# Kernel tuning notes

Hardware: AMD Instinct MI355X
Metric: run time of the kernel (lower is better)

The kernel has to match this reference:

```python
import jax, jax.numpy as jnp
import numpy as np

B, N, D_IN, D, K, H, ITERS = 128, 4096, 64, 64, 8, 128, 3
SCALE = D ** -0.5
EPS_ATTN = 1e-8
EPS_LN = 1e-5


def layer_norm(x, g, b):
    m = jnp.mean(x, axis=-1, keepdims=True)
    v = jnp.mean((x - m) ** 2, axis=-1, keepdims=True)
    return (x - m) * jax.lax.rsqrt(v + EPS_LN) * g + b


def setup_inputs() -> dict:
    key = jax.random.key(0)
    ks = jax.random.split(key, 16)
    s = 0.05
    return {
        "inputs": jax.random.normal(ks[0], (B, N, D_IN), dtype=jnp.float32),
        "noise": jax.random.normal(ks[1], (B, K, D), dtype=jnp.float32),
        "slots_mu": jax.random.normal(ks[2], (1, 1, D), dtype=jnp.float32),
        "slots_sigma": jax.random.normal(ks[3], (1, 1, D), dtype=jnp.float32),
        "Wq": jax.random.normal(ks[4], (D, D), dtype=jnp.float32) * s,
        "Wk": jax.random.normal(ks[5], (D_IN, D), dtype=jnp.float32) * s,
        "Wv": jax.random.normal(ks[6], (D_IN, D), dtype=jnp.float32) * s,
        "W_ih": jax.random.normal(ks[7], (3 * D, D), dtype=jnp.float32) * s,
        "W_hh": jax.random.normal(ks[8], (3 * D, D), dtype=jnp.float32) * s,
        "b_ih": jnp.zeros((3 * D,), dtype=jnp.float32),
        "b_hh": jnp.zeros((3 * D,), dtype=jnp.float32),
        "mlp_W1": jax.random.normal(ks[9], (D, H), dtype=jnp.float32) * s,
        "mlp_b1": jnp.zeros((H,), dtype=jnp.float32),
        "mlp_W2": jax.random.normal(ks[10], (H, D), dtype=jnp.float32) * s,
        "mlp_b2": jnp.zeros((D,), dtype=jnp.float32),
        "ln_in_g": jnp.ones((D_IN,), dtype=jnp.float32),
        "ln_in_b": jnp.zeros((D_IN,), dtype=jnp.float32),
        "ln_s_g": jnp.ones((D,), dtype=jnp.float32),
        "ln_s_b": jnp.zeros((D,), dtype=jnp.float32),
        "ln_ff_g": jnp.ones((D,), dtype=jnp.float32),
        "ln_ff_b": jnp.zeros((D,), dtype=jnp.float32),
    }


def reference(inputs, noise, slots_mu, slots_sigma, Wq, Wk, Wv,
              W_ih, W_hh, b_ih, b_hh, mlp_W1, mlp_b1, mlp_W2, mlp_b2,
              ln_in_g, ln_in_b, ln_s_g, ln_s_b, ln_ff_g, ln_ff_b):
    # slots = Normal(mu, sigma) with externally supplied standard noise
    slots = slots_mu + slots_sigma * noise                      # [B,K,D]
    x = layer_norm(inputs, ln_in_g, ln_in_b)                     # [B,N,D_IN]
    k = x @ Wk                                                   # [B,N,D]
    v = x @ Wv                                                   # [B,N,D]

    for _ in range(ITERS):
        slots_prev = slots
        s = layer_norm(slots, ln_s_g, ln_s_b)
        q = s @ Wq                                               # [B,K,D]
        dots = jnp.einsum('bid,bjd->bij', q, k) * SCALE          # [B,K,N]
        attn = jax.nn.softmax(dots, axis=1) + EPS_ATTN           # softmax over slots
        attn_n = attn / jnp.sum(attn, axis=-1, keepdims=True)
        updates = jnp.einsum('bjd,bij->bid', v, attn_n)          # [B,K,D]

        # single-step GRU (torch nn.GRU gate order: reset, update, new)
        gx = updates @ W_ih.T + b_ih                             # [B,K,3D]
        gh = slots_prev @ W_hh.T + b_hh                          # [B,K,3D]
        gx_r, gx_z, gx_n = jnp.split(gx, 3, axis=-1)
        gh_r, gh_z, gh_n = jnp.split(gh, 3, axis=-1)
        r = jax.nn.sigmoid(gx_r + gh_r)
        z = jax.nn.sigmoid(gx_z + gh_z)
        n = jnp.tanh(gx_n + r * gh_n)
        slots = (1.0 - z) * n + z * slots_prev

        slots = layer_norm(slots, ln_ff_g, ln_ff_b)
        slots = slots + (jax.nn.relu(slots @ mlp_W1 + mlp_b1) @ mlp_W2 + mlp_b2)
    return slots
```

## Files before the change

kernel.cpp:

```cpp
#include <hip/hip_runtime.h>
#include <hip/hip_bf16.h>

typedef unsigned int u32;
typedef unsigned short u16;
typedef __attribute__((ext_vector_type(8))) short short8;
typedef __attribute__((ext_vector_type(4))) float f32x4;
typedef __attribute__((ext_vector_type(2))) u32 u32x2;

#define B_      128
#define N_      4096
#define K_      8
#define ITERS_  3
#define OC_     8
#define CPB_    4
#define CHUNK   128
#define SCALE_  0.125f
#define EPS_A   1e-8f
#define EPS_LN  1e-5f

__device__ __forceinline__ float bf_lo(u32 u){ union{u32 v; float f;} x; x.v = u<<16; return x.f; }
__device__ __forceinline__ u16 f2bf(float f){
  union{float f; u32 v;} x; x.f = f;
  u32 v = x.v;
  return (u16)((v + 0x7fffu + ((v>>16)&1u))>>16);
}
__device__ __forceinline__ float wsum64(float v){
  #pragma unroll
  for (int off=32; off; off>>=1) v += __shfl_xor(v, off, 64);
  return v;
}
__device__ __forceinline__ void gll16(const void* g, void* l){
  __builtin_amdgcn_global_load_lds(
      (const __attribute__((address_space(1))) void*)g,
      (__attribute__((address_space(3))) void*)l, 16, 0, 0);
}

__global__ void prep_t(const float* __restrict__ Wih, const float* __restrict__ Whh,
                       const float* __restrict__ Wq,  const float* __restrict__ Wk,
                       float* __restrict__ WihT, float* __restrict__ WhhT,
                       float* __restrict__ Wqk){
  int t = threadIdx.x;
  if (blockIdx.x < 48){
    int idx = blockIdx.x*256 + t;
    int g = idx>>6, d = idx&63;
    WihT[d*192+g] = Wih[idx];
    WhhT[d*192+g] = Whh[idx];
  } else {
    __shared__ float WkL[64*65];
    int bi = blockIdx.x - 48;
    #pragma unroll
    for (int k=0;k<16;++k){
      int idx = t + k*256;
      int d = idx>>6, m = idx&63;
      WkL[m*65+d] = Wk[idx];
    }
    __syncthreads();
    int a = bi*4 + (t>>6), d = t&63;
    float acc = 0.f;
    #pragma unroll 8
    for (int m=0;m<64;++m) acc += Wq[a*64+m]*WkL[m*65+d];
    Wqk[a*64+d] = acc;
  }
}

__global__ __launch_bounds__(512) void slots_init(
    const float* __restrict__ noise, const float* __restrict__ mu, const float* __restrict__ sigma,
    const float* __restrict__ Wqk,
    const float* __restrict__ lnsg, const float* __restrict__ lnsb,
    float* __restrict__ slots, u16* __restrict__ qbuf16){
  int b = blockIdx.x, t = threadIdx.x;
  int i = t>>6, d = t&63;
  __shared__ float svL[K_][68];
  float s0 = mu[d] + sigma[d]*noise[b*512 + t];
  slots[b*512 + t] = s0;
  float m  = wsum64(s0) * (1.f/64.f);
  float df = s0 - m;
  float vv = wsum64(df*df) * (1.f/64.f);
  float sv = df * rsqrtf(vv + EPS_LN) * lnsg[d] + lnsb[d];
  svL[i][d] = sv;
  __syncthreads();
  float qt = 0.f;
  #pragma unroll 8
  for (int dd=0; dd<64; ++dd) qt += svL[i][dd] * Wqk[dd*64 + d];
  qbuf16[b*1024 + t] = f2bf(qt);
  qbuf16[b*1024 + 512 + t] = 0;
}

template<int FUSED>
__global__ __launch_bounds__(256,4) void bigpass(
    const float* __restrict__ inp, u16* __restrict__ xhat,
    const u16* __restrict__ qbuf16,
    const float* __restrict__ lng, const float* __restrict__ lnb,
    float* __restrict__ PU, float* __restrict__ PS){
  int b = blockIdx.y, oc = blockIdx.x, t = threadIdx.x;
  int w = t>>6, lane = t&63;
  int fr = lane&15, fq = lane>>4;

  __shared__ __align__(16) char smem[38912];
  char* qA   = smem + 32768;
  char* abuf = smem + 34816;
  __shared__ float SL[4][8];
  u32 smb = (u32)(size_t)smem;

  if (t < 128){
    uint4 v = ((const uint4*)(qbuf16 + b*1024))[t];
    int row = t>>3;
    *(uint4*)(qA + ((t*16) ^ ((row&7)<<4))) = v;
  }
  long tile0 = ((long)b*OC_ + oc)*CPB_;
  long base_pos = (long)b*N_ + (long)oc*(CPB_*CHUNK);

  short8 qf0, qf1;
  f32x4 c2 = (f32x4){0.f,0.f,0.f,0.f};
  float tsl[4] = {0.f,0.f,0.f,0.f};

  float lg[16], lb[16];
  if (FUSED){
    int q = t&3;
    #pragma unroll
    for (int e=0;e<16;++e){ lg[e] = lng[q*16+e]; lb[e] = lnb[q*16+e]; }
  }
  if (!FUSED){
    const char* gsrc = (const char*)xhat + (tile0<<14) + w*4096 + lane*16;
    char* ldst = smem + w*4096;
    #pragma unroll
    for (int j=0;j<4;++j) gll16(gsrc + j*1024, ldst + j*1024);
  }

  #pragma unroll
  for (int cc=0; cc<CPB_; ++cc){
    int buf = cc&1;
    if (FUSED){
      #pragma unroll
      for (int p2=0;p2<2;++p2){
        int r = p2*64 + (t>>2), q = t&3;
        const float4* xr = (const float4*)(inp + (base_pos + (long)cc*CHUNK + r)*64 + q*16);
        float xv[16]; float s=0.f, sq=0.f;
        #pragma unroll
        for (int c=0;c<4;++c){
          float4 f = xr[c];
          xv[c*4+0]=f.x; xv[c*4+1]=f.y; xv[c*4+2]=f.z; xv[c*4+3]=f.w;
          s  += f.x+f.y+f.z+f.w;
          sq += f.x*f.x+f.y*f.y+f.z*f.z+f.w*f.w;
        }
        s  += __shfl_xor(s,1,64);  s  += __shfl_xor(s,2,64);
        sq += __shfl_xor(sq,1,64); sq += __shfl_xor(sq,2,64);
        float mean = s*(1.f/64.f);
        float inv  = rsqrtf(sq*(1.f/64.f) - mean*mean + EPS_LN);
        u32 pk[8];
        #pragma unroll
        for (int e=0;e<8;++e){
          float a0 = (xv[e*2]  -mean)*inv*lg[e*2]   + lb[e*2];
          float a1 = (xv[e*2+1]-mean)*inv*lg[e*2+1] + lb[e*2+1];
          pk[e] = (u32)f2bf(a0) | ((u32)f2bf(a1)<<16);
        }
        uint4 v0; v0.x=pk[0]; v0.y=pk[1]; v0.z=pk[2]; v0.w=pk[3];
        uint4 v1; v1.x=pk[4]; v1.y=pk[5]; v1.z=pk[6]; v1.w=pk[7];
        int byte0 = ((r>>5)<<12) | (q<<10) | (((r>>2)&1)<<9) | (((r>>3)&3)<<7) | ((r&3)<<5);
        *(uint4*)(smem + buf*16384 + byte0)      = v0;
        *(uint4*)(smem + buf*16384 + byte0 + 16) = v1;
      }
    }
    __syncthreads();
    if (FUSED){
      const uint4* ls = (const uint4*)(smem + buf*16384);
      uint4* gim = (uint4*)((char*)xhat + ((tile0+cc)<<14));
      #pragma unroll
      for (int j=0;j<4;++j) gim[t + j*256] = ls[t + j*256];
    } else if (cc+1 < CPB_){
      const char* gsrc = (const char*)xhat + ((tile0+cc+1)<<14) + w*4096 + lane*16;
      char* ldst = smem + (buf^1)*16384 + w*4096;
      #pragma unroll
      for (int j=0;j<4;++j) gll16(gsrc + j*1024, ldst + j*1024);
    }
    if (cc==0){
      qf0 = *(const short8*)(qA + ((fr*128 +  0 + fq*16) ^ ((fr&7)<<4)));
      qf1 = *(const short8*)(qA + ((fr*128 + 64 + fq*16) ^ ((fr&7)<<4)));
    }
    f32x4 c1[2];
    #pragma unroll
    for (int nt=0;nt<2;++nt){
      c1[nt] = (f32x4){0.f,0.f,0.f,0.f};
      #pragma unroll
      for (int kk=0;kk<2;++kk){
        int byte = (w<<12) | ((kk*2+(fq>>1))<<10) | (((fr>>2)&1)<<9)
                 | ((nt*2+(fr>>3))<<7) | ((fr&3)<<5) | ((fq&1)<<4);
        short8 xf = *(const short8*)(smem + buf*16384 + byte);
        c1[nt] = __builtin_amdgcn_mfma_f32_16x16x32_bf16(kk?qf1:qf0, xf, c1[nt], 0,0,0);
      }
    }
    #pragma unroll
    for (int nt=0;nt<2;++nt){
      float d0 = c1[nt][0]*SCALE_, d1 = c1[nt][1]*SCALE_;
      float d2 = c1[nt][2]*SCALE_, d3 = c1[nt][3]*SCALE_;
      float m = fmaxf(fmaxf(d0,d1), fmaxf(d2,d3));
      m = fmaxf(m, __shfl_xor(m, 16, 64));
      float e0 = __expf(d0-m), e1 = __expf(d1-m), e2 = __expf(d2-m), e3 = __expf(d3-m);
      float sl = e0+e1+e2+e3;
      float inv = 1.f/(sl + __shfl_xor(sl, 16, 64));
      float a0 = e0*inv + EPS_A, a1 = e1*inv + EPS_A;
      float a2 = e2*inv + EPS_A, a3 = e3*inv + EPS_A;
      tsl[0]+=a0; tsl[1]+=a1; tsl[2]+=a2; tsl[3]+=a3;
      int pos2 = w*64 + nt*32 + fr*2;
      #pragma unroll
      for (int r=0;r<4;++r){
        int slot = fq*4 + r;
        float av = (r==0)?a0:((r==1)?a1:((r==2)?a2:a3));
        int byteA = ((slot<<8) + pos2) ^ ((slot&7)<<4);
        *(u16*)(abuf + byteA) = f2bf(av);
      }
    }
    __syncthreads();
    {
      u32 va = smb + buf*16384 + (w<<10) + (fq<<7) + (fr<<1);
      u32x2 tv0,tv1,tv2,tv3,tv4,tv5,tv6,tv7;
      asm volatile("ds_read_b64_tr_b16 %0, %1 offset:0"     : "=v"(tv0) : "v"(va));
      asm volatile("ds_read_b64_tr_b16 %0, %1 offset:512"   : "=v"(tv1) : "v"(va));
      asm volatile("ds_read_b64_tr_b16 %0, %1 offset:4096"  : "=v"(tv2) : "v"(va));
      asm volatile("ds_read_b64_tr_b16 %0, %1 offset:4608"  : "=v"(tv3) : "v"(va));
      asm volatile("ds_read_b64_tr_b16 %0, %1 offset:8192"  : "=v"(tv4) : "v"(va));
      asm volatile("ds_read_b64_tr_b16 %0, %1 offset:8704"  : "=v"(tv5) : "v"(va));
      asm volatile("ds_read_b64_tr_b16 %0, %1 offset:12288" : "=v"(tv6) : "v"(va));
      asm volatile("ds_read_b64_tr_b16 %0, %1 offset:12800" : "=v"(tv7) : "v"(va));
      short8 pa[4];
      #pragma unroll
      for (int k2=0;k2<4;++k2){
        int byteP = (fr<<8) + ((k2*64 + fq*16) ^ ((fr&7)<<4));
        pa[k2] = *(const short8*)(abuf + byteP);
      }
      asm volatile("s_waitcnt lgkmcnt(0)" ::: "memory");
      __builtin_amdgcn_sched_barrier(0);
      union { short8 s8; u32 u4[4]; } xb;
      xb.u4[0]=tv0.x; xb.u4[1]=tv0.y; xb.u4[2]=tv1.x; xb.u4[3]=tv1.y;
      c2 = __builtin_amdgcn_mfma_f32_16x16x32_bf16(pa[0], xb.s8, c2, 0,0,0);
      xb.u4[0]=tv2.x; xb.u4[1]=tv2.y; xb.u4[2]=tv3.x; xb.u4[3]=tv3.y;
      c2 = __builtin_amdgcn_mfma_f32_16x16x32_bf16(pa[1], xb.s8, c2, 0,0,0);
      xb.u4[0]=tv4.x; xb.u4[1]=tv4.y; xb.u4[2]=tv5.x; xb.u4[3]=tv5.y;
      c2 = __builtin_amdgcn_mfma_f32_16x16x32_bf16(pa[2], xb.s8, c2, 0,0,0);
      xb.u4[0]=tv6.x; xb.u4[1]=tv6.y; xb.u4[2]=tv7.x; xb.u4[3]=tv7.y;
      c2 = __builtin_amdgcn_mfma_f32_16x16x32_bf16(pa[3], xb.s8, c2, 0,0,0);
    }
  }
  long pb = ((long)b*OC_ + oc)*512;
  if (fq < 2){
    #pragma unroll
    for (int r=0;r<4;++r)
      PU[pb + (fq*4+r)*64 + w*16 + fr] = c2[r];
  }
  #pragma unroll
  for (int mk=1; mk<16; mk<<=1){
    tsl[0] += __shfl_xor(tsl[0], mk, 64);
    tsl[1] += __shfl_xor(tsl[1], mk, 64);
    tsl[2] += __shfl_xor(tsl[2], mk, 64);
    tsl[3] += __shfl_xor(tsl[3], mk, 64);
  }
  if (fr==0 && fq<2){
    SL[w][fq*4+0]=tsl[0]; SL[w][fq*4+1]=tsl[1];
    SL[w][fq*4+2]=tsl[2]; SL[w][fq*4+3]=tsl[3];
  }
  __syncthreads();
  if (t < 8)
    PS[((long)b*OC_ + oc)*8 + t] = SL[0][t]+SL[1][t]+SL[2][t]+SL[3][t];
}

__global__ __launch_bounds__(512,2) void slot_update(
    const float* __restrict__ PU, const float* __restrict__ PS,
    float* __restrict__ slots,
    const float* __restrict__ WihT, const float* __restrict__ WhhT,
    const float* __restrict__ bih, const float* __restrict__ bhh,
    const float* __restrict__ W1, const float* __restrict__ b1,
    const float* __restrict__ W2, const float* __restrict__ b2,
    const float* __restrict__ lnffg, const float* __restrict__ lnffb,
    const float* __restrict__ lnsg, const float* __restrict__ lnsb,
    const float* __restrict__ Wv, const float* __restrict__ Wqk,
    u16* __restrict__ qbuf16, float* __restrict__ dout, int last){
  extern __shared__ float wls[];
  __shared__ float updL[K_][68];
  __shared__ float spL[K_][68];
  __shared__ float sfL[K_][68];
  __shared__ float hL[K_][132];
  int b = blockIdx.x, t = threadIdx.x;
  int i = t>>6, d = t&63;
  float u=0.f;
  #pragma unroll
  for (int c=0;c<OC_;++c) u += PU[((long)b*OC_ + c)*512 + t];
  float S=0.f;
  #pragma unroll
  for (int c=0;c<OC_;++c) S += PS[((long)b*OC_ + c)*8 + i];
  float ut = u / S;
  float sp = slots[b*512 + t];
  sfL[i][d] = ut;
  spL[i][d] = sp;
  {
    const float4* wa = (const float4*)WihT;
    #pragma unroll
    for (int k2=0;k2<6;++k2){ int idx = t + k2*512; ((float4*)wls)[idx] = wa[idx]; }
  }
  __syncthreads();
  float upd = 0.f;
  #pragma unroll 8
  for (int dd=0; dd<64; ++dd) upd += sfL[i][dd]*Wv[dd*64 + d];
  updL[i][d] = upd;
  __syncthreads();
  float gx0 = bih[d], gx1 = bih[64+d], gx2 = bih[128+d];
  #pragma unroll 8
  for (int dd=0; dd<64; ++dd){
    float uv = updL[i][dd];
    gx0 += uv*wls[dd*192 + d];
    gx1 += uv*wls[dd*192 + 64 + d];
    gx2 += uv*wls[dd*192 + 128 + d];
  }
  __syncthreads();
  {
    const float4* wb = (const float4*)WhhT;
    #pragma unroll
    for (int k2=0;k2<6;++k2){ int idx = t + k2*512; ((float4*)wls)[idx] = wb[idx]; }
  }
  __syncthreads();
  float gh0 = bhh[d], gh1 = bhh[64+d], gh2 = bhh[128+d];
  #pragma unroll 8
  for (int dd=0; dd<64; ++dd){
    float sv = spL[i][dd];
    gh0 += sv*wls[dd*192 + d];
    gh1 += sv*wls[dd*192 + 64 + d];
    gh2 += sv*wls[dd*192 + 128 + d];
  }
  float rg = 1.f/(1.f+__expf(-(gx0+gh0)));
  float zg = 1.f/(1.f+__expf(-(gx1+gh1)));
  float ng = tanhf(gx2 + rg*gh2);
  float sn = (1.f-zg)*ng + zg*sp;
  float m1 = wsum64(sn)*(1.f/64.f);
  float df = sn-m1;
  float vv = wsum64(df*df)*(1.f/64.f);
  float sf = df*rsqrtf(vv+EPS_LN)*lnffg[d] + lnffb[d];
  sfL[i][d] = sf;
  __syncthreads();
  float h0 = b1[d], h1 = b1[64+d];
  #pragma unroll 8
  for (int dd=0;dd<64;++dd){
    float sv = sfL[i][dd];
    h0 += sv*W1[dd*128 + d];
    h1 += sv*W1[dd*128 + 64 + d];
  }
  h0 = fmaxf(h0, 0.f); h1 = fmaxf(h1, 0.f);
  hL[i][d] = h0; hL[i][d+64] = h1;
  __syncthreads();
  float o = b2[d];
  #pragma unroll 8
  for (int hh=0; hh<128; ++hh) o += hL[i][hh]*W2[hh*64 + d];
  float out = sf + o;
  slots[b*512 + t] = out;
  if (last){
    dout[b*512 + t] = out;
  } else {
    float m2 = wsum64(out)*(1.f/64.f);
    float d2 = out-m2;
    float v2 = wsum64(d2*d2)*(1.f/64.f);
    float sq = d2*rsqrtf(v2+EPS_LN)*lnsg[d] + lnsb[d];
    updL[i][d] = sq;
    __syncthreads();
    float qt=0.f;
    #pragma unroll 8
    for (int dd=0;dd<64;++dd) qt += updL[i][dd]*Wqk[dd*64 + d];
    qbuf16[b*1024 + t] = f2bf(qt);
    qbuf16[b*1024 + 512 + t] = 0;
  }
}

extern "C" void kernel_launch(void* const* d_in, const int* in_sizes, int n_in,
                              void* d_out, int out_size, void* d_ws, size_t ws_size,
                              hipStream_t stream){
  const float* inp   = (const float*)d_in[0];
  const float* noise = (const float*)d_in[1];
  const float* mu    = (const float*)d_in[2];
  const float* sigma = (const float*)d_in[3];
  const float* Wq    = (const float*)d_in[4];
  const float* Wk    = (const float*)d_in[5];
  const float* Wv    = (const float*)d_in[6];
  const float* Wih   = (const float*)d_in[7];
  const float* Whh   = (const float*)d_in[8];
  const float* bih   = (const float*)d_in[9];
  const float* bhh   = (const float*)d_in[10];
  const float* W1    = (const float*)d_in[11];
  const float* b1    = (const float*)d_in[12];
  const float* W2    = (const float*)d_in[13];
  const float* b2    = (const float*)d_in[14];
  const float* lnig  = (const float*)d_in[15];
  const float* lnib  = (const float*)d_in[16];
  const float* lnsg  = (const float*)d_in[17];
  const float* lnsb  = (const float*)d_in[18];
  const float* lnffg = (const float*)d_in[19];
  const float* lnffb = (const float*)d_in[20];
  float* out = (float*)d_out;

  char* ws = (char*)d_ws;
  u16*   xhat   = (u16*)(ws);
  u16*   qbuf16 = (u16*)(ws + 67108864);
  float* slots  = (float*)(ws + 67371008);
  float* PU     = (float*)(ws + 67633152);
  float* PS     = (float*)(ws + 69730304);
  float* WihT   = (float*)(ws + 69763072);
  float* WhhT   = (float*)(ws + 69812224);
  float* Wqk    = (float*)(ws + 69861376);

  prep_t<<<64,256,0,stream>>>(Wih, Whh, Wq, Wk, WihT, WhhT, Wqk);
  slots_init<<<B_,512,0,stream>>>(noise, mu, sigma, Wqk, lnsg, lnsb, slots, qbuf16);
  for (int it=0; it<ITERS_; ++it){
    if (it==0)
      bigpass<1><<<dim3(OC_,B_),256,0,stream>>>(inp, xhat, qbuf16, lnig, lnib, PU, PS);
    else
      bigpass<0><<<dim3(OC_,B_),256,0,stream>>>(inp, xhat, qbuf16, lnig, lnib, PU, PS);
    slot_update<<<B_,512,49152,stream>>>(PU, PS, slots, WihT, WhhT, bih, bhh,
                                     W1, b1, W2, b2, lnffg, lnffb, lnsg, lnsb,
                                     Wv, Wqk, qbuf16, out, (it==ITERS_-1)?1:0);
  }
}
```

Baseline: 160.0 us.

## Make each wavefront own its own position chunks, removing block-wide barriers

```diff
diff --git a/kernel.cpp b/kernel.cpp
--- a/kernel.cpp
+++ b/kernel.cpp
@@ -11,9 +11,7 @@
 #define N_      4096
 #define K_      8
 #define ITERS_  3
-#define OC_     8
-#define CPB_    4
-#define CHUNK   128
+#define NW_     32
 #define SCALE_  0.125f
 #define EPS_A   1e-8f
 #define EPS_LN  1e-5f
@@ -95,97 +93,104 @@
   int b = blockIdx.y, oc = blockIdx.x, t = threadIdx.x;
   int w = t>>6, lane = t&63;
   int fr = lane&15, fq = lane>>4;
-
-  __shared__ __align__(16) char smem[38912];
-  char* qA   = smem + 32768;
-  char* abuf = smem + 34816;
-  __shared__ float SL[4][8];
-  u32 smb = (u32)(size_t)smem;
-
-  if (t < 128){
-    uint4 v = ((const uint4*)(qbuf16 + b*1024))[t];
-    int row = t>>3;
-    *(uint4*)(qA + ((t*16) ^ ((row&7)<<4))) = v;
-  }
-  long tile0 = ((long)b*OC_ + oc)*CPB_;
-  long base_pos = (long)b*N_ + (long)oc*(CPB_*CHUNK);
-
-  short8 qf0, qf1;
-  f32x4 c2 = (f32x4){0.f,0.f,0.f,0.f};
+  int wv = oc*4 + w;
+
+  __shared__ __align__(16) char smem[36864];
+  char* wbase = smem + w*9216;
+  char* abuf  = wbase + 8192;
+  u32 smb = (u32)(size_t)wbase;
+
+  long tile0 = (long)b*128 + wv*4;
+
+  const u16* qb = qbuf16 + b*1024;
+  short8 qf0 = *(const short8*)(qb + fr*64 +      fq*8);
+  short8 qf1 = *(const short8*)(qb + fr*64 + 32 + fq*8);
+
+  f32x4 c2[4];
+  #pragma unroll
+  for (int i=0;i<4;++i) c2[i] = (f32x4){0.f,0.f,0.f,0.f};
   float tsl[4] = {0.f,0.f,0.f,0.f};
 
-  float lg[16], lb[16];
-  if (FUSED){
-    int q = t&3;
-    #pragma unroll
-    for (int e=0;e<16;++e){ lg[e] = lng[q*16+e]; lb[e] = lnb[q*16+e]; }
-  }
   if (!FUSED){
-    const char* gsrc = (const char*)xhat + (tile0<<14) + w*4096 + lane*16;
-    char* ldst = smem + w*4096;
-    #pragma unroll
-    for (int j=0;j<4;++j) gll16(gsrc + j*1024, ldst + j*1024);
+    const char* g0 = (const char*)xhat + (tile0<<12) + lane*16;
+    #pragma unroll
+    for (int j=0;j<4;++j) gll16(g0 + j*1024, wbase + j*1024);
   }
 
   #pragma unroll
-  for (int cc=0; cc<CPB_; ++cc){
-    int buf = cc&1;
-    if (FUSED){
-      #pragma unroll
-      for (int p2=0;p2<2;++p2){
-        int r = p2*64 + (t>>2), q = t&3;
-        const float4* xr = (const float4*)(inp + (base_pos + (long)cc*CHUNK + r)*64 + q*16);
-        float xv[16]; float s=0.f, sq=0.f;
+  for (int cc=0; cc<4; ++cc){
+    int buf = FUSED ? 0 : (cc&1);
+    char* ibuf = wbase + buf*4096;
+    if (!FUSED){
+      if (cc < 3){
+        const char* gn = (const char*)xhat + ((tile0+cc+1)<<12) + lane*16;
+        char* ln = wbase + ((cc+1)&1)*4096;
         #pragma unroll
-        for (int c=0;c<4;++c){
-          float4 f = xr[c];
-          xv[c*4+0]=f.x; xv[c*4+1]=f.y; xv[c*4+2]=f.z; xv[c*4+3]=f.w;
-          s  += f.x+f.y+f.z+f.w;
-          sq += f.x*f.x+f.y*f.y+f.z*f.z+f.w*f.w;
-        }
-        s  += __shfl_xor(s,1,64);  s  += __shfl_xor(s,2,64);
-        sq += __shfl_xor(sq,1,64); sq += __shfl_xor(sq,2,64);
-        float mean = s*(1.f/64.f);
-        float inv  = rsqrtf(sq*(1.f/64.f) - mean*mean + EPS_LN);
-        u32 pk[8];
+        for (int j=0;j<4;++j) gll16(gn + j*1024, ln + j*1024);
+        asm volatile("s_waitcnt vmcnt(4)" ::: "memory");
+      } else {
+        asm volatile("s_waitcnt vmcnt(0)" ::: "memory");
+      }
+      __builtin_amdgcn_sched_barrier(0);
+    } else {
+      int r = lane>>1, h = lane&1;
+      const float4* xr = (const float4*)(inp + ((long)b*N_ + wv*128 + cc*32 + r)*64 + h*32);
+      float xv[32]; float s=0.f, sq=0.f;
+      #pragma unroll
+      for (int c=0;c<8;++c){
+        float4 f = xr[c];
+        xv[c*4+0]=f.x; xv[c*4+1]=f.y; xv[c*4+2]=f.z; xv[c*4+3]=f.w;
+        s  += f.x+f.y+f.z+f.w;
+        sq += f.x*f.x+f.y*f.y+f.z*f.z+f.w*f.w;
+      }
+      s  += __shfl_xor(s,1,64);
+      sq += __shfl_xor(sq,1,64);
+      float mean = s*(1.f/64.f);
+      float inv  = rsqrtf(sq*(1.f/64.f) - mean*mean + EPS_LN);
+      float lgv[32], lbv[32];
+      {
+        const float4* g4 = (const float4*)(lng + h*32);
+        const float4* b4 = (const float4*)(lnb + h*32);
         #pragma unroll
         for (int e=0;e<8;++e){
-          float a0 = (xv[e*2]  -mean)*inv*lg[e*2]   + lb[e*2];
-          float a1 = (xv[e*2+1]-mean)*inv*lg[e*2+1] + lb[e*2+1];
-          pk[e] = (u32)f2bf(a0) | ((u32)f2bf(a1)<<16);
+          float4 gv = g4[e], bv = b4[e];
+          lgv[e*4+0]=gv.x; lgv[e*4+1]=gv.y; lgv[e*4+2]=gv.z; lgv[e*4+3]=gv.w;
+          lbv[e*4+0]=bv.x; lbv[e*4+1]=bv.y; lbv[e*4+2]=bv.z; lbv[e*4+3]=bv.w;
         }
-        uint4 v0; v0.x=pk[0]; v0.y=pk[1]; v0.z=pk[2]; v0.w=pk[3];
-        uint4 v1; v1.x=pk[4]; v1.y=pk[5]; v1.z=pk[6]; v1.w=pk[7];
-        int byte0 = ((r>>5)<<12) | (q<<10) | (((r>>2)&1)<<9) | (((r>>3)&3)<<7) | ((r&3)<<5);
-        *(uint4*)(smem + buf*16384 + byte0)      = v0;
-        *(uint4*)(smem + buf*16384 + byte0 + 16) = v1;
-      }
-    }
-    __syncthreads();
-    if (FUSED){
-      const uint4* ls = (const uint4*)(smem + buf*16384);
-      uint4* gim = (uint4*)((char*)xhat + ((tile0+cc)<<14));
-      #pragma unroll
-      for (int j=0;j<4;++j) gim[t + j*256] = ls[t + j*256];
-    } else if (cc+1 < CPB_){
-      const char* gsrc = (const char*)xhat + ((tile0+cc+1)<<14) + w*4096 + lane*16;
-      char* ldst = smem + (buf^1)*16384 + w*4096;
-      #pragma unroll
-      for (int j=0;j<4;++j) gll16(gsrc + j*1024, ldst + j*1024);
-    }
-    if (cc==0){
-      qf0 = *(const short8*)(qA + ((fr*128 +  0 + fq*16) ^ ((fr&7)<<4)));
-      qf1 = *(const short8*)(qA + ((fr*128 + 64 + fq*16) ^ ((fr&7)<<4)));
-    }
+      }
+      u32 pk[16];
+      #pragma unroll
+      for (int e=0;e<16;++e){
+        float a0 = (xv[e*2]  -mean)*inv*lgv[e*2]   + lbv[e*2];
+        float a1 = (xv[e*2+1]-mean)*inv*lgv[e*2+1] + lbv[e*2+1];
+        pk[e] = (u32)f2bf(a0) | ((u32)f2bf(a1)<<16);
+      }
+      int pbits = (((r>>2)&1)<<9) | (((r>>3)&3)<<7) | ((r&3)<<5);
+      #pragma unroll
+      for (int half=0; half<2; ++half){
+        int dt = h*2 + half;
+        uint4 v0; v0.x=pk[half*8+0]; v0.y=pk[half*8+1]; v0.z=pk[half*8+2]; v0.w=pk[half*8+3];
+        uint4 v1; v1.x=pk[half*8+4]; v1.y=pk[half*8+5]; v1.z=pk[half*8+6]; v1.w=pk[half*8+7];
+        *(uint4*)(ibuf + ((dt<<10) | pbits))      = v0;
+        *(uint4*)(ibuf + ((dt<<10) | pbits) + 16) = v1;
+      }
+      asm volatile("s_waitcnt lgkmcnt(0)" ::: "memory");
+      __builtin_amdgcn_sched_barrier(0);
+      char* gim = (char*)xhat + ((tile0+cc)<<12) + lane*16;
+      #pragma unroll
+      for (int j=0;j<4;++j)
+        *(uint4*)(gim + j*1024) = *(const uint4*)(ibuf + lane*16 + j*1024);
+    }
+
     f32x4 c1[2];
     #pragma unroll
     for (int nt=0;nt<2;++nt){
       c1[nt] = (f32x4){0.f,0.f,0.f,0.f};
       #pragma unroll
       for (int kk=0;kk<2;++kk){
-        int byte = (w<<12) | ((kk*2+(fq>>1))<<10) | (((fr>>2)&1)<<9)
+        int byte = ((kk*2+(fq>>1))<<10) | (((fr>>2)&1)<<9)
                  | ((nt*2+(fr>>3))<<7) | ((fr&3)<<5) | ((fq&1)<<4);
-        short8 xf = *(const short8*)(smem + buf*16384 + byte);
+        short8 xf = *(const short8*)(ibuf + byte);
         c1[nt] = __builtin_amdgcn_mfma_f32_16x16x32_bf16(kk?qf1:qf0, xf, c1[nt], 0,0,0);
       }
     }
@@ -201,51 +206,47 @@
       float a0 = e0*inv + EPS_A, a1 = e1*inv + EPS_A;
       float a2 = e2*inv + EPS_A, a3 = e3*inv + EPS_A;
       tsl[0]+=a0; tsl[1]+=a1; tsl[2]+=a2; tsl[3]+=a3;
-      int pos2 = w*64 + nt*32 + fr*2;
-      #pragma unroll
-      for (int r=0;r<4;++r){
-        int slot = fq*4 + r;
-        float av = (r==0)?a0:((r==1)?a1:((r==2)?a2:a3));
-        int byteA = ((slot<<8) + pos2) ^ ((slot&7)<<4);
-        *(u16*)(abuf + byteA) = f2bf(av);
-      }
-    }
-    __syncthreads();
+      int pos2 = (nt*16 + fr)*2;
+      *(u16*)(abuf + (((fq*4+0)*64 + pos2) ^ (0<<4))) = f2bf(a0);
+      *(u16*)(abuf + (((fq*4+1)*64 + pos2) ^ (1<<4))) = f2bf(a1);
+      *(u16*)(abuf + (((fq*4+2)*64 + pos2) ^ (2<<4))) = f2bf(a2);
+      *(u16*)(abuf + (((fq*4+3)*64 + pos2) ^ (3<<4))) = f2bf(a3);
+    }
+    asm volatile("s_waitcnt lgkmcnt(0)" ::: "memory");
+    __builtin_amdgcn_sched_barrier(0);
     {
-      u32 va = smb + buf*16384 + (w<<10) + (fq<<7) + (fr<<1);
+      short8 pa = *(const short8*)(abuf + ((fr*64 + fq*16) ^ ((fr&3)<<4)));
+      u32 va = smb + buf*4096 + (fq<<7) + (fr<<1);
       u32x2 tv0,tv1,tv2,tv3,tv4,tv5,tv6,tv7;
-      asm volatile("ds_read_b64_tr_b16 %0, %1 offset:0"     : "=v"(tv0) : "v"(va));
-      asm volatile("ds_read_b64_tr_b16 %0, %1 offset:512"   : "=v"(tv1) : "v"(va));
-      asm volatile("ds_read_b64_tr_b16 %0, %1 offset:4096"  : "=v"(tv2) : "v"(va));
-      asm volatile("ds_read_b64_tr_b16 %0, %1 offset:4608"  : "=v"(tv3) : "v"(va));
-      asm volatile("ds_read_b64_tr_b16 %0, %1 offset:8192"  : "=v"(tv4) : "v"(va));
-      asm volatile("ds_read_b64_tr_b16 %0, %1 offset:8704"  : "=v"(tv5) : "v"(va));
-      asm volatile("ds_read_b64_tr_b16 %0, %1 offset:12288" : "=v"(tv6) : "v"(va));
-      asm volatile("ds_read_b64_tr_b16 %0, %1 offset:12800" : "=v"(tv7) : "v"(va));
-      short8 pa[4];
-      #pragma unroll
-      for (int k2=0;k2<4;++k2){
-        int byteP = (fr<<8) + ((k2*64 + fq*16) ^ ((fr&7)<<4));
-        pa[k2] = *(const short8*)(abuf + byteP);
-      }
+      asm volatile("ds_read_b64_tr_b16 %0, %1 offset:0"    : "=v"(tv0) : "v"(va));
+      asm volatile("ds_read_b64_tr_b16 %0, %1 offset:512"  : "=v"(tv1) : "v"(va));
+      asm volatile("ds_read_b64_tr_b16 %0, %1 offset:1024" : "=v"(tv2) : "v"(va));
+      asm volatile("ds_read_b64_tr_b16 %0, %1 offset:1536" : "=v"(tv3) : "v"(va));
+      asm volatile("ds_read_b64_tr_b16 %0, %1 offset:2048" : "=v"(tv4) : "v"(va));
+      asm volatile("ds_read_b64_tr_b16 %0, %1 offset:2560" : "=v"(tv5) : "v"(va));
+      asm volatile("ds_read_b64_tr_b16 %0, %1 offset:3072" : "=v"(tv6) : "v"(va));
+      asm volatile("ds_read_b64_tr_b16 %0, %1 offset:3584" : "=v"(tv7) : "v"(va));
       asm volatile("s_waitcnt lgkmcnt(0)" ::: "memory");
       __builtin_amdgcn_sched_barrier(0);
       union { short8 s8; u32 u4[4]; } xb;
       xb.u4[0]=tv0.x; xb.u4[1]=tv0.y; xb.u4[2]=tv1.x; xb.u4[3]=tv1.y;
-      c2 = __builtin_amdgcn_mfma_f32_16x16x32_bf16(pa[0], xb.s8, c2, 0,0,0);
+      c2[0] = __builtin_amdgcn_mfma_f32_16x16x32_bf16(pa, xb.s8, c2[0], 0,0,0);
       xb.u4[0]=tv2.x; xb.u4[1]=tv2.y; xb.u4[2]=tv3.x; xb.u4[3]=tv3.y;
-      c2 = __builtin_amdgcn_mfma_f32_16x16x32_bf16(pa[1], xb.s8, c2, 0,0,0);
+      c2[1] = __builtin_amdgcn_mfma_f32_16x16x32_bf16(pa, xb.s8, c2[1], 0,0,0);
       xb.u4[0]=tv4.x; xb.u4[1]=tv4.y; xb.u4[2]=tv5.x; xb.u4[3]=tv5.y;
-      c2 = __builtin_amdgcn_mfma_f32_16x16x32_bf16(pa[2], xb.s8, c2, 0,0,0);
+      c2[2] = __builtin_amdgcn_mfma_f32_16x16x32_bf16(pa, xb.s8, c2[2], 0,0,0);
       xb.u4[0]=tv6.x; xb.u4[1]=tv6.y; xb.u4[2]=tv7.x; xb.u4[3]=tv7.y;
-      c2 = __builtin_amdgcn_mfma_f32_16x16x32_bf16(pa[3], xb.s8, c2, 0,0,0);
-    }
-  }
-  long pb = ((long)b*OC_ + oc)*512;
+      c2[3] = __builtin_amdgcn_mfma_f32_16x16x32_bf16(pa, xb.s8, c2[3], 0,0,0);
+    }
+  }
+  long pb = ((long)b*NW_ + wv)*512;
   if (fq < 2){
     #pragma unroll
-    for (int r=0;r<4;++r)
-      PU[pb + (fq*4+r)*64 + w*16 + fr] = c2[r];
+    for (int dblk=0;dblk<4;++dblk){
+      #pragma unroll
+      for (int r=0;r<4;++r)
+        PU[pb + (fq*4+r)*64 + dblk*16 + fr] = c2[dblk][r];
+    }
   }
   #pragma unroll
   for (int mk=1; mk<16; mk<<=1){
@@ -255,12 +256,9 @@
     tsl[3] += __shfl_xor(tsl[3], mk, 64);
   }
   if (fr==0 && fq<2){
-    SL[w][fq*4+0]=tsl[0]; SL[w][fq*4+1]=tsl[1];
-    SL[w][fq*4+2]=tsl[2]; SL[w][fq*4+3]=tsl[3];
-  }
-  __syncthreads();
-  if (t < 8)
-    PS[((long)b*OC_ + oc)*8 + t] = SL[0][t]+SL[1][t]+SL[2][t]+SL[3][t];
+    float* psb = PS + ((long)b*NW_ + wv)*8 + fq*4;
+    psb[0]=tsl[0]; psb[1]=tsl[1]; psb[2]=tsl[2]; psb[3]=tsl[3];
+  }
 }
 
 __global__ __launch_bounds__(512,2) void slot_update(
@@ -282,11 +280,11 @@
   int b = blockIdx.x, t = threadIdx.x;
   int i = t>>6, d = t&63;
   float u=0.f;
-  #pragma unroll
-  for (int c=0;c<OC_;++c) u += PU[((long)b*OC_ + c)*512 + t];
+  #pragma unroll 8
+  for (int c=0;c<NW_;++c) u += PU[((long)b*NW_ + c)*512 + t];
   float S=0.f;
-  #pragma unroll
-  for (int c=0;c<OC_;++c) S += PS[((long)b*OC_ + c)*8 + i];
+  #pragma unroll 8
+  for (int c=0;c<NW_;++c) S += PS[((long)b*NW_ + c)*8 + i];
   float ut = u / S;
   float sp = slots[b*512 + t];
   sfL[i][d] = ut;
@@ -398,18 +396,18 @@
   u16*   qbuf16 = (u16*)(ws + 67108864);
   float* slots  = (float*)(ws + 67371008);
   float* PU     = (float*)(ws + 67633152);
-  float* PS     = (float*)(ws + 69730304);
-  float* WihT   = (float*)(ws + 69763072);
-  float* WhhT   = (float*)(ws + 69812224);
-  float* Wqk    = (float*)(ws + 69861376);
+  float* PS     = (float*)(ws + 76021760);
+  float* WihT   = (float*)(ws + 76152832);
+  float* WhhT   = (float*)(ws + 76201984);
+  float* Wqk    = (float*)(ws + 76251136);
 
   prep_t<<<64,256,0,stream>>>(Wih, Whh, Wq, Wk, WihT, WhhT, Wqk);
   slots_init<<<B_,512,0,stream>>>(noise, mu, sigma, Wqk, lnsg, lnsb, slots, qbuf16);
   for (int it=0; it<ITERS_; ++it){
     if (it==0)
-      bigpass<1><<<dim3(OC_,B_),256,0,stream>>>(inp, xhat, qbuf16, lnig, lnib, PU, PS);
+      bigpass<1><<<dim3(8,B_),256,0,stream>>>(inp, xhat, qbuf16, lnig, lnib, PU, PS);
     else
-      bigpass<0><<<dim3(OC_,B_),256,0,stream>>>(inp, xhat, qbuf16, lnig, lnib, PU, PS);
+      bigpass<0><<<dim3(8,B_),256,0,stream>>>(inp, xhat, qbuf16, lnig, lnib, PU, PS);
     slot_update<<<B_,512,49152,stream>>>(PU, PS, slots, WihT, WhhT, bih, bhh,
                                      W1, b1, W2, b2, lnffg, lnffb, lnsg, lnsb,
                                      Wv, Wqk, qbuf16, out, (it==ITERS_-1)?1:0);
```

Measured after the change: 185.9 us. 16.2% more time.
